# Kernel tuning notes

Measured on AMD Instinct MI355X. Metric: run time of the kernel, lower is better.

## Reference

```python
import jax, jax.numpy as jnp
import numpy as np

B, S, H, NH = 2, 2048, 1024, 16
HD = H // NH
SCALE = float(H) ** 0.5  # note: source scales by sqrt(hidden_dim), not sqrt(head_dim)
EPS = 1e-5


def setup_inputs() -> dict:
    key = jax.random.key(0)
    ks = jax.random.split(key, 16)
    s = 0.02
    return {
        "q": jax.random.normal(ks[0], (B, S, H), jnp.float32),
        "k": jax.random.normal(ks[1], (B, S, H), jnp.float32),
        "v": jax.random.normal(ks[2], (B, S, H), jnp.float32),
        "mask": jax.random.randint(ks[3], (B, 1, S, S), 0, 2, jnp.int32),
        "Wq": jax.random.normal(ks[4], (H, H), jnp.float32) * s,
        "bq": jnp.zeros((H,), jnp.float32),
        "Wk": jax.random.normal(ks[5], (H, H), jnp.float32) * s,
        "bk": jnp.zeros((H,), jnp.float32),
        "Wv": jax.random.normal(ks[6], (H, H), jnp.float32) * s,
        "bv": jnp.zeros((H,), jnp.float32),
        "Wfc": jax.random.normal(ks[7], (H, H), jnp.float32) * s,
        "bfc": jnp.zeros((H,), jnp.float32),
        "gamma": jnp.ones((H,), jnp.float32),
        "beta": jnp.zeros((H,), jnp.float32),
    }


def reference(q, k, v, mask, Wq, bq, Wk, bk, Wv, bv, Wfc, bfc, gamma, beta):
    residual = q
    qh = (q @ Wq + bq).reshape(B, S, NH, HD)
    kh = (k @ Wk + bk).reshape(B, S, NH, HD)
    vh = (v @ Wv + bv).reshape(B, S, NH, HD)
    # full [B, NH, S, S] score matrix, as in the source
    energy = jnp.einsum('nqhd,nkhd->nhqk', qh, kh)
    energy = jnp.where(mask == 0, jnp.float32(-1e9), energy)
    attn = jax.nn.softmax(energy / SCALE, axis=3)  # dropout p=0.0 -> identity
    out = jnp.einsum('nhqk,nkhd->nqhd', attn, vh).reshape(B, S, H)
    y = out @ Wfc + bfc + residual
    mu = jnp.mean(y, axis=-1, keepdims=True)
    var = jnp.mean((y - mu) ** 2, axis=-1, keepdims=True)
    return gamma * (y - mu) / jnp.sqrt(var + EPS) + beta
```

## Files before the change

### kernel.cpp

```cpp
#include <hip/hip_runtime.h>
#include <hip/hip_bf16.h>

#define S_LEN  2048
#define HDIM   1024
#define NHEADS 16
#define HEADD  64
#define BATCH  2
#define MTOT   (BATCH * S_LEN)
#define K2EXP  0.04508422f

typedef __attribute__((ext_vector_type(8)))  __bf16 bf16x8;
typedef __attribute__((ext_vector_type(4)))  __bf16 bf16x4;
typedef __attribute__((ext_vector_type(4)))  float  f32x4;
typedef __attribute__((ext_vector_type(16))) float  f32x16;

__device__ __forceinline__ void gload16(const void* g, void* l) {
  __builtin_amdgcn_global_load_lds(
      (const __attribute__((address_space(1))) void*)g,
      (__attribute__((address_space(3))) void*)l, 16, 0, 0);
}
template<int STRIDE>
__device__ __forceinline__ bf16x8 lds_rdS(const __bf16* base, int row, int bcol) {
  const char* p = (const char*)base + row * STRIDE + (bcol ^ ((row & (STRIDE / 16 - 1)) << 4));
  return *(const bf16x8*)p;
}
__device__ __forceinline__ unsigned cvtpk_bf16(float lo, float hi) {
  unsigned r;
  asm("v_cvt_pk_bf16_f32 %0, %1, %2" : "=v"(r) : "v"(lo), "v"(hi));
  return r;
}
__device__ __forceinline__ void plswap(unsigned& a, unsigned& b) {
  asm volatile("v_permlane32_swap_b32 %0, %1" : "+v"(a), "+v"(b));
}

__global__ __launch_bounds__(256)
void prologue_kernel(const float* __restrict__ q, const float* __restrict__ k,
                     const float* __restrict__ v, const int* __restrict__ mask,
                     const float* __restrict__ Wq, const float* __restrict__ Wk,
                     const float* __restrict__ Wv, const float* __restrict__ Wfc,
                     __bf16* __restrict__ Qc, __bf16* __restrict__ Kc,
                     __bf16* __restrict__ Vc, unsigned* __restrict__ mbH,
                     __bf16* __restrict__ Wt)
{
  __shared__ float T[64][65];
  const int id = blockIdx.x;
  const int tid = threadIdx.x;
  if (id < 6144) {
    const int z = id >> 11, blk = id & 2047;
    const float* src = (z == 0) ? q : (z == 1) ? k : v;
    __bf16* dst = (z == 0) ? Qc : (z == 1) ? Kc : Vc;
    const size_t i = ((size_t)blk * 256 + tid) * 8;
    const float4 a = *(const float4*)&src[i];
    const float4 c = *(const float4*)&src[i + 4];
    bf16x8 o;
    o[0] = (__bf16)a.x; o[1] = (__bf16)a.y; o[2] = (__bf16)a.z; o[3] = (__bf16)a.w;
    o[4] = (__bf16)c.x; o[5] = (__bf16)c.y; o[6] = (__bf16)c.z; o[7] = (__bf16)c.w;
    *(bf16x8*)&dst[i] = o;
  } else if (id < 38912) {
    const size_t idx = (size_t)(id - 6144) * 256 + tid;
    const int m = mask[idx];
    const unsigned long long bal = __ballot(m != 0);
    const int lane = tid & 63;
    if ((lane & 31) == 0) {
      const int hh = lane >> 5;
      unsigned wlo = 0, whi = 0;
      #pragma unroll
      for (int j = 0; j < 16; ++j) {
        const int kvl = (j & 3) + 8 * (j >> 2) + 4 * hh;
        wlo |= (unsigned)((bal >> kvl) & 1ULL) << j;
        whi |= (unsigned)((bal >> (32 + kvl)) & 1ULL) << j;
      }
      const int b   = (int)(idx >> 22);
      const int qq  = (int)(idx >> 11) & 2047;
      const int seg = ((int)idx & 2047) >> 6;
      mbH[(((size_t)(hh * 2 + b)) * 32 + seg) * S_LEN + qq] = wlo | (whi << 16);
    }
  } else {
    const int f = id - 38912;
    const int z = f >> 8;
    const float* W = (z == 0) ? Wq : (z == 1) ? Wk : (z == 2) ? Wv : Wfc;
    const float sc = (z == 0) ? K2EXP : 1.0f;
    __bf16* O = Wt + (size_t)z * HDIM * HDIM;
    const int k0 = ((f >> 4) & 15) * 64, n0 = (f & 15) * 64;
    const int r  = tid >> 4;
    const int c4 = (tid & 15) * 4;
    #pragma unroll
    for (int p = 0; p < 4; ++p) {
      const int row = r + p * 16;
      const float4 vv = *(const float4*)&W[(size_t)(k0 + row) * HDIM + n0 + c4];
      T[row][c4 + 0] = vv.x; T[row][c4 + 1] = vv.y;
      T[row][c4 + 2] = vv.z; T[row][c4 + 3] = vv.w;
    }
    __syncthreads();
    #pragma unroll
    for (int p = 0; p < 4; ++p) {
      const int n = r + p * 16;
      bf16x4 o;
      #pragma unroll
      for (int i = 0; i < 4; ++i) o[i] = (__bf16)(T[c4 + i][n] * sc);
      *(bf16x4*)&O[(size_t)(n0 + n) * HDIM + k0 + c4] = o;
    }
  }
}

template<int MODE, int BMT>
__device__ __forceinline__ void gemm_body(
    __bf16* As, __bf16* Bs,
    const __bf16* __restrict__ A, const __bf16* __restrict__ Wt,
    const float* __restrict__ bias, float bscale,
    const float* __restrict__ resid,
    __bf16* __restrict__ Ob, float* __restrict__ Of, __bf16* __restrict__ Vtg)
{
  constexpr int AI = BMT / 32;
  const int tid = threadIdx.x, lane = tid & 63, w = tid >> 6;
  const int fr = lane & 15, k8 = (lane >> 4) * 8;
  const int wr = w >> 1, wc = w & 1;
  const int f   = blockIdx.x + gridDim.x * blockIdx.y;
  const int cpx = (gridDim.x * gridDim.y) >> 3;
  const int fs  = (f & 7) * cpx + (f >> 3);
  const int m0 = (fs / gridDim.x) * BMT, n0 = (fs % gridDim.x) * 128;
  const int srow8 = lane >> 3, slot = lane & 7;

  f32x4 acc[AI][4] = {};

  #define G_STAGE(kt, bf)                                                    \
    {                                                                        \
      _Pragma("unroll")                                                      \
      for (int c = 0; c < AI; ++c) {                                         \
        const int ra = w * (BMT / 4) + c * 8 + srow8;                        \
        gload16(&A[(size_t)(m0 + ra) * HDIM + (kt) * 64 + ((slot ^ (ra & 7)) * 8)], \
                (void*)&As[((bf) * BMT + ra) * 64]);                         \
      }                                                                      \
      _Pragma("unroll")                                                      \
      for (int c = 0; c < 4; ++c) {                                          \
        const int rb = w * 32 + c * 8 + srow8;                               \
        gload16(&Wt[(size_t)(n0 + rb) * HDIM + (kt) * 64 + ((slot ^ (rb & 7)) * 8)], \
                (void*)&Bs[((bf) * 128 + rb) * 64]);                         \
      }                                                                      \
    }

  #define G_COMPUTE(bf)                                                      \
    {                                                                        \
      _Pragma("unroll")                                                      \
      for (int kk = 0; kk < 64; kk += 32) {                                  \
        bf16x8 a[AI], b[4];                                                  \
        _Pragma("unroll")                                                    \
        for (int i = 0; i < AI; ++i)                                         \
          a[i] = lds_rdS<128>(&As[(bf) * BMT * 64], wr * (BMT / 2) + i * 16 + fr, (kk + k8) * 2); \
        _Pragma("unroll")                                                    \
        for (int j = 0; j < 4; ++j)                                          \
          b[j] = lds_rdS<128>(&Bs[(bf) * 128 * 64], wc * 64 + j * 16 + fr, (kk + k8) * 2); \
        _Pragma("unroll")                                                    \
        for (int i = 0; i < AI; ++i)                                         \
          _Pragma("unroll")                                                  \
          for (int j = 0; j < 4; ++j)                                        \
            acc[i][j] = __builtin_amdgcn_mfma_f32_16x16x32_bf16(a[i], b[j], acc[i][j], 0, 0, 0); \
      }                                                                      \
    }

  G_STAGE(0, 0)
  for (int kt = 0; kt < 15; ++kt) {
    G_STAGE(kt + 1, (kt + 1) & 1)
    if constexpr (BMT == 128) asm volatile("s_waitcnt vmcnt(8)" ::: "memory");
    else                      asm volatile("s_waitcnt vmcnt(6)" ::: "memory");
    __builtin_amdgcn_s_barrier();
    __builtin_amdgcn_sched_barrier(0);
    __builtin_amdgcn_s_setprio(1);
    G_COMPUTE(kt & 1)
    __builtin_amdgcn_s_setprio(0);
    __builtin_amdgcn_sched_barrier(0);
    __builtin_amdgcn_s_barrier();
  }
  asm volatile("s_waitcnt vmcnt(0)" ::: "memory");
  __builtin_amdgcn_s_barrier();
  G_COMPUTE(1)

  const int rg = (lane >> 4) * 4;
  #pragma unroll
  for (int i = 0; i < AI; ++i) {
    #pragma unroll
    for (int j = 0; j < 4; ++j) {
      const int col = n0 + wc * 64 + j * 16 + fr;
      if constexpr (MODE == 2) {
        const int h = col >> 6, hd = col & 63;
        const int row = m0 + wr * (BMT / 2) + i * 16 + rg;
        const int bq = row >> 11, qq = row & 2047;
        bf16x4 o;
        #pragma unroll
        for (int r = 0; r < 4; ++r) o[r] = (__bf16)(acc[i][j][r] + bias[col]);
        *(bf16x4*)&Vtg[(((size_t)bq * NHEADS + h) * HEADD + hd) * S_LEN + qq] = o;
      } else {
        #pragma unroll
        for (int r = 0; r < 4; ++r) {
          const int row = m0 + wr * (BMT / 2) + i * 16 + rg + r;
          if constexpr (MODE == 0) {
            Ob[(size_t)row * HDIM + col] = (__bf16)(acc[i][j][r] + bias[col] * bscale);
          } else {
            Of[(size_t)row * HDIM + col] =
                acc[i][j][r] + bias[col] + resid[(size_t)row * HDIM + col];
          }
        }
      }
    }
  }
  #undef G_STAGE
  #undef G_COMPUTE
}

__global__ __launch_bounds__(256)
void qkv_kernel(const __bf16* __restrict__ Qc, const __bf16* __restrict__ Kc,
                const __bf16* __restrict__ Vc, const __bf16* __restrict__ Wt,
                const float* __restrict__ bq, const float* __restrict__ bk,
                const float* __restrict__ bv,
                __bf16* __restrict__ Qb, __bf16* __restrict__ Kb,
                __bf16* __restrict__ Vtg)
{
  __shared__ __bf16 smem[2 * 128 * 64 * 2];
  __bf16* As = smem;
  __bf16* Bs = smem + 2 * 128 * 64;
  const int z = blockIdx.z;
  if (z == 2) {
    gemm_body<2, 128>(As, Bs, Vc, Wt + (size_t)2 * HDIM * HDIM, bv, 1.0f,
                      nullptr, nullptr, nullptr, Vtg);
  } else {
    gemm_body<0, 128>(As, Bs, z ? Kc : Qc, Wt + (size_t)z * HDIM * HDIM,
                      z ? bk : bq, z ? 1.0f : K2EXP, nullptr,
                      z ? Kb : Qb, nullptr, nullptr);
  }
}

__global__ __launch_bounds__(256)
void fc_kernel(const __bf16* __restrict__ A, const __bf16* __restrict__ Wt,
               const float* __restrict__ bias, const float* __restrict__ resid,
               float* __restrict__ Of)
{
  __shared__ __bf16 smem[2 * 64 * 64 + 2 * 128 * 64];
  __bf16* As = smem;
  __bf16* Bs = smem + 2 * 64 * 64;
  gemm_body<1, 64>(As, Bs, A, Wt + (size_t)3 * HDIM * HDIM, bias, 1.0f, resid,
                   nullptr, Of, nullptr);
}

__global__ __launch_bounds__(128)
void attn_kernel(const __bf16* __restrict__ Qb, const __bf16* __restrict__ Kb,
                 const __bf16* __restrict__ Vtg, const unsigned* __restrict__ mbH,
                 __bf16* __restrict__ AO)
{
  __shared__ __bf16 Ks[2][64][64];
  __shared__ __bf16 Vt[2][64][64];

  const int bh = blockIdx.x, b = bh >> 4, h = bh & 15;
  const int tid = threadIdx.x, lane = tid & 63, w = tid >> 6;
  const int fr = lane & 31, hi = lane >> 5;
  const int qw = blockIdx.y * 64 + w * 32;
  const int q  = qw + fr;

  bf16x8 qf[4];
  #pragma unroll
  for (int st = 0; st < 4; ++st)
    qf[st] = *(const bf16x8*)&Qb[((size_t)b * S_LEN + q) * HDIM + h * HEADD + st * 16 + hi * 8];

  const int srl = w * 8 + (lane >> 3);
  const int ssw = ((lane & 7) ^ (srl & 7)) * 8;
  const __bf16* ksrc = Kb  + ((size_t)b * S_LEN + srl) * HDIM + h * HEADD + ssw;
  const __bf16* vsrc = Vtg + ((size_t)bh * HEADD + srl) * S_LEN + ssw;
  const unsigned* tbl = mbH + ((size_t)(hi * 2 + b) * 32) * S_LEN + q;

  bf16x8 ones;
  #pragma unroll
  for (int e = 0; e < 8; ++e) ones[e] = (__bf16)1.0f;

  f32x16 o0 = {}, o1 = {}, l_acc = {};
  unsigned mv, nm = 0;

  mv = tbl[0];
  #pragma unroll
  for (int c = 0; c < 4; ++c)
    gload16(ksrc + (size_t)(16 * c) * HDIM, (void*)&Ks[0][c * 16 + w * 8][0]);
  #pragma unroll
  for (int c = 0; c < 4; ++c)
    gload16(vsrc + (size_t)(16 * c) * S_LEN, (void*)&Vt[0][c * 16 + w * 8][0]);

  for (int t = 0; t < 32; ++t) {
    const int buf = t & 1;
    const __bf16* Kbuf = &Ks[buf][0][0];
    const __bf16* Vbuf = &Vt[buf][0][0];
    if (t < 31) {
      nm = tbl[(size_t)(t + 1) * S_LEN];
      const __bf16* kp = ksrc + (size_t)(t + 1) * 64 * HDIM;
      const __bf16* vp = vsrc + (size_t)(t + 1) * 64;
      #pragma unroll
      for (int c = 0; c < 4; ++c)
        gload16(kp + (size_t)(16 * c) * HDIM, (void*)&Ks[buf ^ 1][c * 16 + w * 8][0]);
      #pragma unroll
      for (int c = 0; c < 4; ++c)
        gload16(vp + (size_t)(16 * c) * S_LEN, (void*)&Vt[buf ^ 1][c * 16 + w * 8][0]);
      asm volatile("s_waitcnt vmcnt(8)" ::: "memory");
    } else {
      asm volatile("s_waitcnt vmcnt(0)" ::: "memory");
    }
    __builtin_amdgcn_s_barrier();
    __builtin_amdgcn_sched_barrier(0);

    f32x16 s0 = {}, s1 = {};
    __builtin_amdgcn_s_setprio(1);
    #pragma unroll
    for (int st = 0; st < 4; ++st) {
      s0 = __builtin_amdgcn_mfma_f32_32x32x16_bf16(
          lds_rdS<128>(Kbuf, fr,      st * 32 + hi * 16), qf[st], s0, 0, 0, 0);
      s1 = __builtin_amdgcn_mfma_f32_32x32x16_bf16(
          lds_rdS<128>(Kbuf, 32 + fr, st * 32 + hi * 16), qf[st], s1, 0, 0, 0);
    }
    __builtin_amdgcn_s_setprio(0);

    float pp[32];
    #pragma unroll
    for (int j = 0; j < 16; ++j) {
      const float e0 = __builtin_amdgcn_exp2f(s0[j]);
      const float e1 = __builtin_amdgcn_exp2f(s1[j]);
      const unsigned a0 = (unsigned)((int)(mv << (31 - j)) >> 31);
      const unsigned a1 = (unsigned)((int)(mv << (15 - j)) >> 31);
      pp[j]      = __uint_as_float(a0 & __float_as_uint(e0));
      pp[16 + j] = __uint_as_float(a1 & __float_as_uint(e1));
    }

    bf16x8 pa[4];
    #pragma unroll
    for (int g = 0; g < 4; ++g) {
      const int o = (g >> 1) * 16 + (g & 1) * 8;
      unsigned x  = cvtpk_bf16(pp[o + 0], pp[o + 1]);
      unsigned x2 = cvtpk_bf16(pp[o + 2], pp[o + 3]);
      unsigned y  = cvtpk_bf16(pp[o + 4], pp[o + 5]);
      unsigned y2 = cvtpk_bf16(pp[o + 6], pp[o + 7]);
      plswap(x, y);
      plswap(x2, y2);
      union { unsigned u[4]; bf16x8 v; } uu;
      uu.u[0] = x; uu.u[1] = x2; uu.u[2] = y; uu.u[3] = y2;
      pa[g] = uu.v;
    }

    __builtin_amdgcn_s_setprio(1);
    #pragma unroll
    for (int g = 0; g < 4; ++g) {
      l_acc = __builtin_amdgcn_mfma_f32_32x32x16_bf16(pa[g], ones, l_acc, 0, 0, 0);
      o0 = __builtin_amdgcn_mfma_f32_32x32x16_bf16(
          pa[g], lds_rdS<128>(Vbuf, fr,      g * 32 + hi * 16), o0, 0, 0, 0);
      o1 = __builtin_amdgcn_mfma_f32_32x32x16_bf16(
          pa[g], lds_rdS<128>(Vbuf, 32 + fr, g * 32 + hi * 16), o1, 0, 0, 0);
    }
    __builtin_amdgcn_s_setprio(0);

    mv = nm;
    __builtin_amdgcn_sched_barrier(0);
    __builtin_amdgcn_s_barrier();
  }

  #pragma unroll
  for (int g = 0; g < 4; ++g) {
    #pragma unroll
    for (int r = 0; r < 4; ++r) {
      const int j = g * 4 + r;
      const float inv = __builtin_amdgcn_rcpf(l_acc[j]);
      const int qq = qw + g * 8 + hi * 4 + r;
      AO[((size_t)b * S_LEN + qq) * HDIM + h * HEADD + fr]      = (__bf16)(o0[j] * inv);
      AO[((size_t)b * S_LEN + qq) * HDIM + h * HEADD + 32 + fr] = (__bf16)(o1[j] * inv);
    }
  }
}

__global__ __launch_bounds__(256)
void ln_kernel(float* __restrict__ y, const float* __restrict__ gamma,
               const float* __restrict__ beta)
{
  __shared__ float red[8];
  const int tid = threadIdx.x;
  float* p = y + (size_t)blockIdx.x * HDIM;

  float4 vv = *(const float4*)&p[tid * 4];
  float s  = vv.x + vv.y + vv.z + vv.w;
  float ss = vv.x * vv.x + vv.y * vv.y + vv.z * vv.z + vv.w * vv.w;
  #pragma unroll
  for (int d = 1; d < 64; d <<= 1) {
    s  += __shfl_xor(s, d);
    ss += __shfl_xor(ss, d);
  }
  const int wid = tid >> 6;
  if ((tid & 63) == 0) { red[wid * 2] = s; red[wid * 2 + 1] = ss; }
  __syncthreads();
  s  = red[0] + red[2] + red[4] + red[6];
  ss = red[1] + red[3] + red[5] + red[7];
  const float mean = s * (1.0f / HDIM);
  const float var  = ss * (1.0f / HDIM) - mean * mean;
  const float inv  = rsqrtf(var + 1e-5f);

  const float4 g  = *(const float4*)&gamma[tid * 4];
  const float4 bt = *(const float4*)&beta[tid * 4];
  vv.x = (vv.x - mean) * inv * g.x + bt.x;
  vv.y = (vv.y - mean) * inv * g.y + bt.y;
  vv.z = (vv.z - mean) * inv * g.z + bt.z;
  vv.w = (vv.w - mean) * inv * g.w + bt.w;
  *(float4*)&p[tid * 4] = vv;
}

extern "C" void kernel_launch(void* const* d_in, const int* in_sizes, int n_in,
                              void* d_out, int out_size, void* d_ws, size_t ws_size,
                              hipStream_t stream) {
  const float* q     = (const float*)d_in[0];
  const float* k     = (const float*)d_in[1];
  const float* v     = (const float*)d_in[2];
  const int*   mask  = (const int*)  d_in[3];
  const float* Wq    = (const float*)d_in[4];
  const float* bq    = (const float*)d_in[5];
  const float* Wk    = (const float*)d_in[6];
  const float* bk    = (const float*)d_in[7];
  const float* Wv    = (const float*)d_in[8];
  const float* bv    = (const float*)d_in[9];
  const float* Wfc   = (const float*)d_in[10];
  const float* bfc   = (const float*)d_in[11];
  const float* gamma = (const float*)d_in[12];
  const float* beta  = (const float*)d_in[13];
  float* out = (float*)d_out;

  char* ws = (char*)d_ws;
  const size_t MB16 = (size_t)MTOT * HDIM * 2;
  unsigned* mbH = (unsigned*)ws;
  __bf16* Wt  = (__bf16*)(ws + (1u << 20));
  __bf16* Qc  = (__bf16*)(ws + (1u << 20) + 4 * (size_t)HDIM * HDIM * 2);
  __bf16* Kc  = (__bf16*)((char*)Qc + MB16);
  __bf16* Vc  = (__bf16*)((char*)Kc + MB16);
  __bf16* Qb  = (__bf16*)((char*)Vc + MB16);
  __bf16* Kb  = (__bf16*)((char*)Qb + MB16);
  __bf16* Vtg = (__bf16*)((char*)Kb + MB16);
  __bf16* AO  = Kc;

  const dim3 blk(256);

  prologue_kernel<<<dim3(39936), blk, 0, stream>>>(
      q, k, v, mask, Wq, Wk, Wv, Wfc, Qc, Kc, Vc, mbH, Wt);

  qkv_kernel<<<dim3(HDIM / 128, MTOT / 128, 3), blk, 0, stream>>>(
      Qc, Kc, Vc, Wt, bq, bk, bv, Qb, Kb, Vtg);

  attn_kernel<<<dim3(BATCH * NHEADS, S_LEN / 64), dim3(128), 0, stream>>>(
      Qb, Kb, Vtg, mbH, AO);

  fc_kernel<<<dim3(HDIM / 128, MTOT / 64), blk, 0, stream>>>(
      AO, Wt, bfc, q, out);

  ln_kernel<<<dim3(MTOT), blk, 0, stream>>>(out, gamma, beta);
}
```

Baseline: 167.7 us.

## Triple-buffer K/V tiles in attention and use single barrier per iteration

```diff
diff --git a/kernel.cpp b/kernel.cpp
--- a/kernel.cpp
+++ b/kernel.cpp
@@ -246,8 +246,8 @@
                  const __bf16* __restrict__ Vtg, const unsigned* __restrict__ mbH,
                  __bf16* __restrict__ AO)
 {
-  __shared__ __bf16 Ks[2][64][64];
-  __shared__ __bf16 Vt[2][64][64];
+  __shared__ __bf16 Ks[3][64][64];
+  __shared__ __bf16 Vt[3][64][64];
 
   const int bh = blockIdx.x, b = bh >> 4, h = bh & 15;
   const int tid = threadIdx.x, lane = tid & 63, w = tid >> 6;
@@ -273,34 +273,36 @@
   f32x16 o0 = {}, o1 = {}, l_acc = {};
   unsigned mv, nm = 0;
 
+  #define A_STAGE(tt, sb)                                                    \
+    { const size_t kvo = (size_t)(tt) * 64;                                  \
+      _Pragma("unroll")                                                      \
+      for (int c = 0; c < 4; ++c)                                            \
+        gload16(ksrc + (kvo + 16 * c) * HDIM, (void*)&Ks[sb][c * 16 + w * 8][0]); \
+      _Pragma("unroll")                                                      \
+      for (int c = 0; c < 4; ++c)                                            \
+        gload16(vsrc + kvo + (size_t)(16 * c) * S_LEN, (void*)&Vt[sb][c * 16 + w * 8][0]); }
+
   mv = tbl[0];
-  #pragma unroll
-  for (int c = 0; c < 4; ++c)
-    gload16(ksrc + (size_t)(16 * c) * HDIM, (void*)&Ks[0][c * 16 + w * 8][0]);
-  #pragma unroll
-  for (int c = 0; c < 4; ++c)
-    gload16(vsrc + (size_t)(16 * c) * S_LEN, (void*)&Vt[0][c * 16 + w * 8][0]);
-
+  A_STAGE(0, 0)
+  A_STAGE(1, 1)
+
+  int cb = 0;
   for (int t = 0; t < 32; ++t) {
-    const int buf = t & 1;
-    const __bf16* Kbuf = &Ks[buf][0][0];
-    const __bf16* Vbuf = &Vt[buf][0][0];
-    if (t < 31) {
-      nm = tbl[(size_t)(t + 1) * S_LEN];
-      const __bf16* kp = ksrc + (size_t)(t + 1) * 64 * HDIM;
-      const __bf16* vp = vsrc + (size_t)(t + 1) * 64;
-      #pragma unroll
-      for (int c = 0; c < 4; ++c)
-        gload16(kp + (size_t)(16 * c) * HDIM, (void*)&Ks[buf ^ 1][c * 16 + w * 8][0]);
-      #pragma unroll
-      for (int c = 0; c < 4; ++c)
-        gload16(vp + (size_t)(16 * c) * S_LEN, (void*)&Vt[buf ^ 1][c * 16 + w * 8][0]);
+    __builtin_amdgcn_s_barrier();
+    if (t < 31) nm = tbl[(size_t)(t + 1) * S_LEN];
+    if (t < 30) {
+      const int sb = (cb == 0) ? 2 : cb - 1;
+      A_STAGE(t + 2, sb)
+      asm volatile("s_waitcnt vmcnt(16)" ::: "memory");
+    } else if (t == 30) {
       asm volatile("s_waitcnt vmcnt(8)" ::: "memory");
     } else {
       asm volatile("s_waitcnt vmcnt(0)" ::: "memory");
     }
-    __builtin_amdgcn_s_barrier();
     __builtin_amdgcn_sched_barrier(0);
+
+    const __bf16* Kbuf = &Ks[cb][0][0];
+    const __bf16* Vbuf = &Vt[cb][0][0];
 
     f32x16 s0 = {}, s1 = {};
     __builtin_amdgcn_s_setprio(1);
@@ -318,8 +320,8 @@
     for (int j = 0; j < 16; ++j) {
       const float e0 = __builtin_amdgcn_exp2f(s0[j]);
       const float e1 = __builtin_amdgcn_exp2f(s1[j]);
-      const unsigned a0 = (unsigned)((int)(mv << (31 - j)) >> 31);
-      const unsigned a1 = (unsigned)((int)(mv << (15 - j)) >> 31);
+      const unsigned a0 = (unsigned)__builtin_amdgcn_sbfe(mv, j, 1);
+      const unsigned a1 = (unsigned)__builtin_amdgcn_sbfe(mv, j + 16, 1);
       pp[j]      = __uint_as_float(a0 & __float_as_uint(e0));
       pp[16 + j] = __uint_as_float(a1 & __float_as_uint(e1));
     }
@@ -351,9 +353,9 @@
     __builtin_amdgcn_s_setprio(0);
 
     mv = nm;
-    __builtin_amdgcn_sched_barrier(0);
-    __builtin_amdgcn_s_barrier();
-  }
+    cb = (cb == 2) ? 0 : cb + 1;
+  }
+  #undef A_STAGE
 
   #pragma unroll
   for (int g = 0; g < 4; ++g) {
```

New measurement: 200.5 us. +19.6%, slower.

## Enlarge attention block to 128 queries, single barrier per tile, split softmax halves

Applied to the files above, without the earlier changes.

```diff
diff --git a/kernel.cpp b/kernel.cpp
--- a/kernel.cpp
+++ b/kernel.cpp
@@ -241,7 +241,7 @@
                    nullptr, Of, nullptr);
 }
 
-__global__ __launch_bounds__(128)
+__global__ __launch_bounds__(256)
 void attn_kernel(const __bf16* __restrict__ Qb, const __bf16* __restrict__ Kb,
                  const __bf16* __restrict__ Vtg, const unsigned* __restrict__ mbH,
                  __bf16* __restrict__ AO)
@@ -252,7 +252,7 @@
   const int bh = blockIdx.x, b = bh >> 4, h = bh & 15;
   const int tid = threadIdx.x, lane = tid & 63, w = tid >> 6;
   const int fr = lane & 31, hi = lane >> 5;
-  const int qw = blockIdx.y * 64 + w * 32;
+  const int qw = blockIdx.y * 128 + w * 32;
   const int q  = qw + fr;
 
   bf16x8 qf[4];
@@ -260,7 +260,7 @@
   for (int st = 0; st < 4; ++st)
     qf[st] = *(const bf16x8*)&Qb[((size_t)b * S_LEN + q) * HDIM + h * HEADD + st * 16 + hi * 8];
 
-  const int srl = w * 8 + (lane >> 3);
+  const int srl = w * 16 + (lane >> 3);
   const int ssw = ((lane & 7) ^ (srl & 7)) * 8;
   const __bf16* ksrc = Kb  + ((size_t)b * S_LEN + srl) * HDIM + h * HEADD + ssw;
   const __bf16* vsrc = Vtg + ((size_t)bh * HEADD + srl) * S_LEN + ssw;
@@ -274,33 +274,30 @@
   unsigned mv, nm = 0;
 
   mv = tbl[0];
-  #pragma unroll
-  for (int c = 0; c < 4; ++c)
-    gload16(ksrc + (size_t)(16 * c) * HDIM, (void*)&Ks[0][c * 16 + w * 8][0]);
-  #pragma unroll
-  for (int c = 0; c < 4; ++c)
-    gload16(vsrc + (size_t)(16 * c) * S_LEN, (void*)&Vt[0][c * 16 + w * 8][0]);
+  gload16(ksrc,             (void*)&Ks[0][w * 16][0]);
+  gload16(ksrc + 8 * HDIM,  (void*)&Ks[0][w * 16 + 8][0]);
+  gload16(vsrc,             (void*)&Vt[0][w * 16][0]);
+  gload16(vsrc + 8 * S_LEN, (void*)&Vt[0][w * 16 + 8][0]);
 
   for (int t = 0; t < 32; ++t) {
     const int buf = t & 1;
-    const __bf16* Kbuf = &Ks[buf][0][0];
-    const __bf16* Vbuf = &Vt[buf][0][0];
+    __builtin_amdgcn_s_barrier();
     if (t < 31) {
       nm = tbl[(size_t)(t + 1) * S_LEN];
       const __bf16* kp = ksrc + (size_t)(t + 1) * 64 * HDIM;
       const __bf16* vp = vsrc + (size_t)(t + 1) * 64;
-      #pragma unroll
-      for (int c = 0; c < 4; ++c)
-        gload16(kp + (size_t)(16 * c) * HDIM, (void*)&Ks[buf ^ 1][c * 16 + w * 8][0]);
-      #pragma unroll
-      for (int c = 0; c < 4; ++c)
-        gload16(vp + (size_t)(16 * c) * S_LEN, (void*)&Vt[buf ^ 1][c * 16 + w * 8][0]);
-      asm volatile("s_waitcnt vmcnt(8)" ::: "memory");
+      gload16(kp,             (void*)&Ks[buf ^ 1][w * 16][0]);
+      gload16(kp + 8 * HDIM,  (void*)&Ks[buf ^ 1][w * 16 + 8][0]);
+      gload16(vp,             (void*)&Vt[buf ^ 1][w * 16][0]);
+      gload16(vp + 8 * S_LEN, (void*)&Vt[buf ^ 1][w * 16 + 8][0]);
+      asm volatile("s_waitcnt vmcnt(5)" ::: "memory");
     } else {
       asm volatile("s_waitcnt vmcnt(0)" ::: "memory");
     }
-    __builtin_amdgcn_s_barrier();
     __builtin_amdgcn_sched_barrier(0);
+
+    const __bf16* Kbuf = &Ks[buf][0][0];
+    const __bf16* Vbuf = &Vt[buf][0][0];
 
     f32x16 s0 = {}, s1 = {};
     __builtin_amdgcn_s_setprio(1);
@@ -313,46 +310,75 @@
     }
     __builtin_amdgcn_s_setprio(0);
 
-    float pp[32];
-    #pragma unroll
-    for (int j = 0; j < 16; ++j) {
-      const float e0 = __builtin_amdgcn_exp2f(s0[j]);
-      const float e1 = __builtin_amdgcn_exp2f(s1[j]);
-      const unsigned a0 = (unsigned)((int)(mv << (31 - j)) >> 31);
-      const unsigned a1 = (unsigned)((int)(mv << (15 - j)) >> 31);
-      pp[j]      = __uint_as_float(a0 & __float_as_uint(e0));
-      pp[16 + j] = __uint_as_float(a1 & __float_as_uint(e1));
-    }
-
-    bf16x8 pa[4];
-    #pragma unroll
-    for (int g = 0; g < 4; ++g) {
-      const int o = (g >> 1) * 16 + (g & 1) * 8;
-      unsigned x  = cvtpk_bf16(pp[o + 0], pp[o + 1]);
-      unsigned x2 = cvtpk_bf16(pp[o + 2], pp[o + 3]);
-      unsigned y  = cvtpk_bf16(pp[o + 4], pp[o + 5]);
-      unsigned y2 = cvtpk_bf16(pp[o + 6], pp[o + 7]);
-      plswap(x, y);
-      plswap(x2, y2);
-      union { unsigned u[4]; bf16x8 v; } uu;
-      uu.u[0] = x; uu.u[1] = x2; uu.u[2] = y; uu.u[3] = y2;
-      pa[g] = uu.v;
-    }
-
-    __builtin_amdgcn_s_setprio(1);
-    #pragma unroll
-    for (int g = 0; g < 4; ++g) {
-      l_acc = __builtin_amdgcn_mfma_f32_32x32x16_bf16(pa[g], ones, l_acc, 0, 0, 0);
-      o0 = __builtin_amdgcn_mfma_f32_32x32x16_bf16(
-          pa[g], lds_rdS<128>(Vbuf, fr,      g * 32 + hi * 16), o0, 0, 0, 0);
-      o1 = __builtin_amdgcn_mfma_f32_32x32x16_bf16(
-          pa[g], lds_rdS<128>(Vbuf, 32 + fr, g * 32 + hi * 16), o1, 0, 0, 0);
-    }
-    __builtin_amdgcn_s_setprio(0);
+    {
+      float pp[16];
+      #pragma unroll
+      for (int j = 0; j < 16; ++j) {
+        const float e0 = __builtin_amdgcn_exp2f(s0[j]);
+        const unsigned a0 = (unsigned)__builtin_amdgcn_sbfe(mv, j, 1);
+        pp[j] = __uint_as_float(a0 & __float_as_uint(e0));
+      }
+      bf16x8 pa[2];
+      #pragma unroll
+      for (int g = 0; g < 2; ++g) {
+        const int o = g * 8;
+        unsigned x  = cvtpk_bf16(pp[o + 0], pp[o + 1]);
+        unsigned x2 = cvtpk_bf16(pp[o + 2], pp[o + 3]);
+        unsigned y  = cvtpk_bf16(pp[o + 4], pp[o + 5]);
+        unsigned y2 = cvtpk_bf16(pp[o + 6], pp[o + 7]);
+        plswap(x, y);
+        plswap(x2, y2);
+        union { unsigned u[4]; bf16x8 v; } uu;
+        uu.u[0] = x; uu.u[1] = x2; uu.u[2] = y; uu.u[3] = y2;
+        pa[g] = uu.v;
+      }
+      __builtin_amdgcn_s_setprio(1);
+      #pragma unroll
+      for (int g = 0; g < 2; ++g) {
+        l_acc = __builtin_amdgcn_mfma_f32_32x32x16_bf16(pa[g], ones, l_acc, 0, 0, 0);
+        o0 = __builtin_amdgcn_mfma_f32_32x32x16_bf16(
+            pa[g], lds_rdS<128>(Vbuf, fr,      g * 32 + hi * 16), o0, 0, 0, 0);
+        o1 = __builtin_amdgcn_mfma_f32_32x32x16_bf16(
+            pa[g], lds_rdS<128>(Vbuf, 32 + fr, g * 32 + hi * 16), o1, 0, 0, 0);
+      }
+      __builtin_amdgcn_s_setprio(0);
+    }
+
+    {
+      float pp[16];
+      #pragma unroll
+      for (int j = 0; j < 16; ++j) {
+        const float e1 = __builtin_amdgcn_exp2f(s1[j]);
+        const unsigned a1 = (unsigned)__builtin_amdgcn_sbfe(mv, j + 16, 1);
+        pp[j] = __uint_as_float(a1 & __float_as_uint(e1));
+      }
+      bf16x8 pa[2];
+      #pragma unroll
+      for (int g = 0; g < 2; ++g) {
+        const int o = g * 8;
+        unsigned x  = cvtpk_bf16(pp[o + 0], pp[o + 1]);
+        unsigned x2 = cvtpk_bf16(pp[o + 2], pp[o + 3]);
+        unsigned y  = cvtpk_bf16(pp[o + 4], pp[o + 5]);
+        unsigned y2 = cvtpk_bf16(pp[o + 6], pp[o + 7]);
+        plswap(x, y);
+        plswap(x2, y2);
+        union { unsigned u[4]; bf16x8 v; } uu;
+        uu.u[0] = x; uu.u[1] = x2; uu.u[2] = y; uu.u[3] = y2;
+        pa[g] = uu.v;
+      }
+      __builtin_amdgcn_s_setprio(1);
+      #pragma unroll
+      for (int g = 0; g < 2; ++g) {
+        l_acc = __builtin_amdgcn_mfma_f32_32x32x16_bf16(pa[g], ones, l_acc, 0, 0, 0);
+        o0 = __builtin_amdgcn_mfma_f32_32x32x16_bf16(
+            pa[g], lds_rdS<128>(Vbuf, fr,      (2 + g) * 32 + hi * 16), o0, 0, 0, 0);
+        o1 = __builtin_amdgcn_mfma_f32_32x32x16_bf16(
+            pa[g], lds_rdS<128>(Vbuf, 32 + fr, (2 + g) * 32 + hi * 16), o1, 0, 0, 0);
+      }
+      __builtin_amdgcn_s_setprio(0);
+    }
 
     mv = nm;
-    __builtin_amdgcn_sched_barrier(0);
-    __builtin_amdgcn_s_barrier();
   }
 
   #pragma unroll
@@ -441,7 +467,7 @@
   qkv_kernel<<<dim3(HDIM / 128, MTOT / 128, 3), blk, 0, stream>>>(
       Qc, Kc, Vc, Wt, bq, bk, bv, Qb, Kb, Vtg);
 
-  attn_kernel<<<dim3(BATCH * NHEADS, S_LEN / 64), dim3(128), 0, stream>>>(
+  attn_kernel<<<dim3(BATCH * NHEADS, S_LEN / 128), blk, 0, stream>>>(
       Qb, Kb, Vtg, mbH, AO);
 
   fc_kernel<<<dim3(HDIM / 128, MTOT / 64), blk, 0, stream>>>(
```

New measurement: 160.5 us. -4.3%, faster.
